# Optimization experiments

Measured on AMD Instinct MI355X. Metric: run time of the kernel, lower is better.

## Reference

```python
import jax, jax.numpy as jnp
import numpy as np

KERAS_EPSILON = 1e-7  # keras.backend.epsilon()


def setup_inputs() -> dict:
    key = jax.random.key(0)
    x = jax.random.normal(key, (4, 2048, 128), dtype=jnp.float32)
    return {"x": x}


def reference(x) -> jnp.ndarray:
    # Euclidean distance matrix: D[b, i, j] = sqrt(sum_d (x[b,i,d] - x[b,j,d])^2 + eps)
    # Computed via the ||a||^2 + ||b||^2 - 2 a.b identity to avoid the
    # [B, N, N, D] broadcasted intermediate of the original implementation.
    sq = jnp.sum(x * x, axis=-1)                      # [B, N]
    cross = jnp.einsum("bnd,bmd->bnm", x, x)           # [B, N, N]
    d2 = sq[:, :, None] + sq[:, None, :] - 2.0 * cross  # [B, N, N]
    d2 = jnp.maximum(d2, 0.0)  # clamp tiny negative rounding errors
    return jnp.sqrt(d2 + KERAS_EPSILON)
```

## Files before the change

kernel.cpp:

```cpp
#include <hip/hip_runtime.h>
#include <hip/hip_bf16.h>

typedef __attribute__((ext_vector_type(8))) __bf16 bf16x8;
typedef __attribute__((ext_vector_type(4))) float  f32x4;

constexpr int NN   = 2048;
constexpr int DD   = 128;
constexpr int TI   = 128;
constexpr int TJ   = 64;
constexpr int ROWB = 256;

__device__ __forceinline__ void gload_lds16(const void* g, void* l) {
    __builtin_amdgcn_global_load_lds(
        (const __attribute__((address_space(1))) void*)g,
        (__attribute__((address_space(3))) void*)l, 16, 0, 0);
}

__global__ __launch_bounds__(256)
void edm_prep(const float* __restrict__ x, __bf16* __restrict__ xb,
              float* __restrict__ sq) {
    const int t  = threadIdx.x;
    const int rl = t >> 4;
    const int c  = t & 15;
    const int g  = blockIdx.x * 16 + rl;

    const float4* p = (const float4*)(x + (size_t)g * DD + c * 8);
    const float4 v0 = p[0];
    const float4 v1 = p[1];
    bf16x8 w;
    w[0] = (__bf16)v0.x; w[1] = (__bf16)v0.y;
    w[2] = (__bf16)v0.z; w[3] = (__bf16)v0.w;
    w[4] = (__bf16)v1.x; w[5] = (__bf16)v1.y;
    w[6] = (__bf16)v1.z; w[7] = (__bf16)v1.w;

    float s = 0.f;
    #pragma unroll
    for (int j = 0; j < 8; ++j) { const float f = (float)w[j]; s += f * f; }

    const int byte = (c * 16) ^ ((g & 7) << 4);
    *(bf16x8*)((char*)xb + (size_t)g * ROWB + byte) = w;

    s += __shfl_xor(s, 1);
    s += __shfl_xor(s, 2);
    s += __shfl_xor(s, 4);
    s += __shfl_xor(s, 8);
    if (c == 0) sq[g] = s;
}

__global__ __launch_bounds__(256, 3)
void edm_main(const __bf16* __restrict__ xb, const float* __restrict__ sq,
              float* __restrict__ out) {
    __shared__ __align__(16) char As[TI * ROWB];
    __shared__ __align__(16) char Bs[TJ * ROWB];

    const int t  = threadIdx.x;
    const int jt = blockIdx.x;
    const int it = blockIdx.y;
    const int b  = blockIdx.z;

    const char* xbase = (const char*)xb + (size_t)b * NN * ROWB;
    const char* srcA  = xbase + (size_t)it * TI * ROWB;
    const char* srcB  = xbase + (size_t)jt * TJ * ROWB;

    #pragma unroll
    for (int i = 0; i < 8; ++i) {
        const int off = (t + i * 256) * 16;
        gload_lds16(srcA + off, As + off);
    }
    #pragma unroll
    for (int i = 0; i < 4; ++i) {
        const int off = (t + i * 256) * 16;
        gload_lds16(srcB + off, Bs + off);
    }

    const int wave = t >> 6;
    const int lane = t & 63;
    const int wm = (wave >> 1) * 64;
    const int wn = (wave & 1) * 32;
    const int lm = lane & 15;
    const int q  = lane >> 4;
    const int swz = (lm & 7) << 4;

    const float* sqi = sq + b * NN + it * TI;
    const float* sqj = sq + b * NN + jt * TJ;
    float si[4];
    #pragma unroll
    for (int mf = 0; mf < 4; ++mf) si[mf] = sqi[wm + mf * 16 + lm];
    f32x4 sj[2];
    #pragma unroll
    for (int nf = 0; nf < 2; ++nf)
        sj[nf] = *(const f32x4*)(sqj + wn + nf * 16 + q * 4);

    __syncthreads();

    f32x4 acc[4][2] = {};
    #pragma unroll
    for (int ks = 0; ks < 4; ++ks) {
        const int cb = ks * 64 + q * 16;
        bf16x8 a[4], bb[2];
        #pragma unroll
        for (int mf = 0; mf < 4; ++mf) {
            const int row = wm + mf * 16 + lm;
            a[mf] = *(const bf16x8*)(As + row * ROWB + (cb ^ swz));
        }
        #pragma unroll
        for (int nf = 0; nf < 2; ++nf) {
            const int row = wn + nf * 16 + lm;
            bb[nf] = *(const bf16x8*)(Bs + row * ROWB + (cb ^ swz));
        }
        #pragma unroll
        for (int mf = 0; mf < 4; ++mf)
            #pragma unroll
            for (int nf = 0; nf < 2; ++nf)
                acc[mf][nf] = __builtin_amdgcn_mfma_f32_16x16x32_bf16(
                    bb[nf], a[mf], acc[mf][nf], 0, 0, 0);
    }

    float* outp = out + ((size_t)b * NN + (size_t)it * TI) * NN + (size_t)jt * TJ;
    #pragma unroll
    for (int mf = 0; mf < 4; ++mf) {
        const int i = wm + mf * 16 + lm;
        float* rowp = outp + (size_t)i * NN;
        const float base = si[mf];
        #pragma unroll
        for (int nf = 0; nf < 2; ++nf) {
            f32x4 d;
            #pragma unroll
            for (int r = 0; r < 4; ++r) {
                float d2 = base + sj[nf][r] - 2.0f * acc[mf][nf][r];
                d2 = fmaxf(d2, 0.0f);
                d[r] = sqrtf(d2 + 1e-7f);
            }
            *(f32x4*)(rowp + wn + nf * 16 + q * 4) = d;
        }
    }
}

extern "C" void kernel_launch(void* const* d_in, const int* in_sizes, int n_in,
                              void* d_out, int out_size, void* d_ws, size_t ws_size,
                              hipStream_t stream) {
    const float* x = (const float*)d_in[0];
    float* out = (float*)d_out;
    float*  sqw = (float*)d_ws;
    __bf16* xbw = (__bf16*)((char*)d_ws + 32768);
    edm_prep<<<dim3((4 * NN) / 16), dim3(256), 0, stream>>>(x, xbw, sqw);
    edm_main<<<dim3(NN / TJ, NN / TI, 4), dim3(256), 0, stream>>>(xbw, sqw, out);
}
```

Before: 85.15 us.

## Process four j-tiles per block with register-resident A and double-buffered B

```diff
diff --git a/kernel.cpp b/kernel.cpp
--- a/kernel.cpp
+++ b/kernel.cpp
@@ -1,5 +1,6 @@
 #include <hip/hip_runtime.h>
 #include <hip/hip_bf16.h>
+#include <math.h>
 
 typedef __attribute__((ext_vector_type(8))) __bf16 bf16x8;
 typedef __attribute__((ext_vector_type(4))) float  f32x4;
@@ -8,12 +9,21 @@
 constexpr int DD   = 128;
 constexpr int TI   = 128;
 constexpr int TJ   = 64;
+constexpr int NJI  = 4;
 constexpr int ROWB = 256;
 
 __device__ __forceinline__ void gload_lds16(const void* g, void* l) {
     __builtin_amdgcn_global_load_lds(
         (const __attribute__((address_space(1))) void*)g,
         (__attribute__((address_space(3))) void*)l, 16, 0, 0);
+}
+
+__device__ __forceinline__ float fast_sqrt(float v) {
+#if __has_builtin(__builtin_amdgcn_sqrtf)
+    return __builtin_amdgcn_sqrtf(v);
+#else
+    return sqrtf(v);
+#endif
 }
 
 __global__ __launch_bounds__(256)
@@ -47,20 +57,22 @@
     if (c == 0) sq[g] = s;
 }
 
-__global__ __launch_bounds__(256, 3)
+__global__ __launch_bounds__(256, 2)
 void edm_main(const __bf16* __restrict__ xb, const float* __restrict__ sq,
               float* __restrict__ out) {
     __shared__ __align__(16) char As[TI * ROWB];
-    __shared__ __align__(16) char Bs[TJ * ROWB];
+    __shared__ __align__(16) char Bs[2][TJ * ROWB];
 
-    const int t  = threadIdx.x;
-    const int jt = blockIdx.x;
-    const int it = blockIdx.y;
-    const int b  = blockIdx.z;
+    const int t = threadIdx.x;
+    const int bid = blockIdx.x + (blockIdx.y << 3) + (blockIdx.z << 7);
+    const int w   = ((bid & 7) << 6) + (bid >> 3);
+    const int jg  = w & 7;
+    const int it  = (w >> 3) & 15;
+    const int b   = w >> 7;
 
     const char* xbase = (const char*)xb + (size_t)b * NN * ROWB;
     const char* srcA  = xbase + (size_t)it * TI * ROWB;
-    const char* srcB  = xbase + (size_t)jt * TJ * ROWB;
+    const char* srcB  = xbase + (size_t)(jg * NJI) * TJ * ROWB;
 
     #pragma unroll
     for (int i = 0; i < 8; ++i) {
@@ -70,7 +82,7 @@
     #pragma unroll
     for (int i = 0; i < 4; ++i) {
         const int off = (t + i * 256) * 16;
-        gload_lds16(srcB + off, Bs + off);
+        gload_lds16(srcB + off, (char*)Bs[0] + off);
     }
 
     const int wave = t >> 6;
@@ -81,58 +93,75 @@
     const int q  = lane >> 4;
     const int swz = (lm & 7) << 4;
 
-    const float* sqi = sq + b * NN + it * TI;
-    const float* sqj = sq + b * NN + jt * TJ;
+    const float* sqi  = sq + b * NN + it * TI;
+    const float* sqj0 = sq + b * NN + jg * NJI * TJ;
     float si[4];
     #pragma unroll
     for (int mf = 0; mf < 4; ++mf) si[mf] = sqi[wm + mf * 16 + lm];
-    f32x4 sj[2];
-    #pragma unroll
-    for (int nf = 0; nf < 2; ++nf)
-        sj[nf] = *(const f32x4*)(sqj + wn + nf * 16 + q * 4);
 
     __syncthreads();
 
-    f32x4 acc[4][2] = {};
+    bf16x8 a[4][4];
     #pragma unroll
     for (int ks = 0; ks < 4; ++ks) {
         const int cb = ks * 64 + q * 16;
-        bf16x8 a[4], bb[2];
+        #pragma unroll
+        for (int mf = 0; mf < 4; ++mf)
+            a[ks][mf] = *(const bf16x8*)(As + (wm + mf * 16 + lm) * ROWB + (cb ^ swz));
+    }
+
+    float* outb = out + ((size_t)b * NN + (size_t)it * TI) * NN
+                      + (size_t)(jg * NJI) * TJ;
+
+    #pragma unroll
+    for (int jj = 0; jj < NJI; ++jj) {
+        if (jj < NJI - 1) {
+            const char* nsrc = srcB + (size_t)(jj + 1) * TJ * ROWB;
+            char* ndst = (char*)Bs[(jj + 1) & 1];
+            #pragma unroll
+            for (int i = 0; i < 4; ++i) {
+                const int off = (t + i * 256) * 16;
+                gload_lds16(nsrc + off, ndst + off);
+            }
+        }
+        f32x4 sj[2];
+        #pragma unroll
+        for (int nf = 0; nf < 2; ++nf)
+            sj[nf] = *(const f32x4*)(sqj0 + jj * TJ + wn + nf * 16 + q * 4);
+
+        const char* Bcur = (const char*)Bs[jj & 1];
+        f32x4 acc[4][2] = {};
+        #pragma unroll
+        for (int ks = 0; ks < 4; ++ks) {
+            const int cb = ks * 64 + q * 16;
+            bf16x8 bb[2];
+            #pragma unroll
+            for (int nf = 0; nf < 2; ++nf)
+                bb[nf] = *(const bf16x8*)(Bcur + (wn + nf * 16 + lm) * ROWB + (cb ^ swz));
+            #pragma unroll
+            for (int mf = 0; mf < 4; ++mf)
+                #pragma unroll
+                for (int nf = 0; nf < 2; ++nf)
+                    acc[mf][nf] = __builtin_amdgcn_mfma_f32_16x16x32_bf16(
+                        bb[nf], a[ks][mf], acc[mf][nf], 0, 0, 0);
+        }
+
         #pragma unroll
         for (int mf = 0; mf < 4; ++mf) {
-            const int row = wm + mf * 16 + lm;
-            a[mf] = *(const bf16x8*)(As + row * ROWB + (cb ^ swz));
+            const int i = wm + mf * 16 + lm;
+            float* rowp = outb + (size_t)i * NN + jj * TJ;
+            #pragma unroll
+            for (int nf = 0; nf < 2; ++nf) {
+                f32x4 d;
+                #pragma unroll
+                for (int r = 0; r < 4; ++r) {
+                    float d2 = si[mf] + sj[nf][r] - 2.0f * acc[mf][nf][r];
+                    d[r] = fast_sqrt(fmaxf(d2, 0.0f) + 1e-7f);
+                }
+                *(f32x4*)(rowp + wn + nf * 16 + q * 4) = d;
+            }
         }
-        #pragma unroll
-        for (int nf = 0; nf < 2; ++nf) {
-            const int row = wn + nf * 16 + lm;
-            bb[nf] = *(const bf16x8*)(Bs + row * ROWB + (cb ^ swz));
-        }
-        #pragma unroll
-        for (int mf = 0; mf < 4; ++mf)
-            #pragma unroll
-            for (int nf = 0; nf < 2; ++nf)
-                acc[mf][nf] = __builtin_amdgcn_mfma_f32_16x16x32_bf16(
-                    bb[nf], a[mf], acc[mf][nf], 0, 0, 0);
-    }
-
-    float* outp = out + ((size_t)b * NN + (size_t)it * TI) * NN + (size_t)jt * TJ;
-    #pragma unroll
-    for (int mf = 0; mf < 4; ++mf) {
-        const int i = wm + mf * 16 + lm;
-        float* rowp = outp + (size_t)i * NN;
-        const float base = si[mf];
-        #pragma unroll
-        for (int nf = 0; nf < 2; ++nf) {
-            f32x4 d;
-            #pragma unroll
-            for (int r = 0; r < 4; ++r) {
-                float d2 = base + sj[nf][r] - 2.0f * acc[mf][nf][r];
-                d2 = fmaxf(d2, 0.0f);
-                d[r] = sqrtf(d2 + 1e-7f);
-            }
-            *(f32x4*)(rowp + wn + nf * 16 + q * 4) = d;
-        }
+        __syncthreads();
     }
 }
 
@@ -144,5 +173,5 @@
     float*  sqw = (float*)d_ws;
     __bf16* xbw = (__bf16*)((char*)d_ws + 32768);
     edm_prep<<<dim3((4 * NN) / 16), dim3(256), 0, stream>>>(x, xbw, sqw);
-    edm_main<<<dim3(NN / TJ, NN / TI, 4), dim3(256), 0, stream>>>(xbw, sqw, out);
+    edm_main<<<dim3(NN / (TJ * NJI), NN / TI, 4), dim3(256), 0, stream>>>(xbw, sqw, out);
 }
```

Result: faster. 80.29 us (-5.7%).
